# Kernel optimization log

Measured on AMD Instinct MI355X. Metric: run time of the kernel, lower is better.

## Reference

```python
import jax, jax.numpy as jnp
import numpy as np

H, W, C_IN, C_OUT, N = 512, 512, 256, 256, 65536


def setup_inputs() -> dict:
    key = jax.random.key(0)
    k1, k2, k3, k4 = jax.random.split(key, 4)
    feature = jax.random.normal(k1, (1, C_IN, H, W), dtype=jnp.float32)
    weight = jax.random.normal(k2, (C_OUT, C_IN, 3, 3), dtype=jnp.float32) * 0.05
    # base sparse locations in the unpadded map; build 3x3 neighborhood indices
    # into the PADDED ([H+2, W+2]) map, exactly like F.pad + fancy indexing.
    base_h = jax.random.randint(k3, (N,), 0, H, dtype=jnp.int32)
    base_w = jax.random.randint(k4, (N,), 0, W, dtype=jnp.int32)
    dh = jnp.repeat(jnp.arange(3, dtype=jnp.int32), 3)  # [9]: 0,0,0,1,1,1,2,2,2
    dw = jnp.tile(jnp.arange(3, dtype=jnp.int32), 3)    # [9]: 0,1,2,0,1,2,...
    h_idx = base_h[None, :] + dh[:, None]  # [9, N], values in [0, H+1]
    w_idx = base_w[None, :] + dw[:, None]  # [9, N], values in [0, W+1]
    return {"feature": feature, "weight": weight, "h_idx": h_idx, "w_idx": w_idx}


def reference(feature, weight, h_idx, w_idx):
    # feature: [1, C, H, W]; weight: [Cout, C, 3, 3]; h_idx/w_idx: [9, N]
    C = feature.shape[1]
    out_ch = weight.shape[0]
    # F.pad(feature, [1,1,1,1])[0] -> [C, H+2, W+2]
    padded = jnp.pad(feature, ((0, 0), (0, 0), (1, 1), (1, 1)))[0]
    # gather 3x3 neighborhoods at sparse locations -> [C, 9, N]
    gathered = padded[:, h_idx, w_idx]
    # .view(9*C, -1): contiguous reshape gives row index c*9 + k
    g = gathered.reshape(C * 9, -1)  # [C*9, N]
    # kernel_d2s = weight.view(out, -1): row ordering c*9 + (kh*3+kw) matches
    k2d = weight.reshape(out_ch, -1)  # [Cout, C*9]
    return k2d @ g  # [Cout, N]
```

## Files before the change

kernel.cpp:

```cpp
#include <hip/hip_runtime.h>
#include <hip/hip_bf16.h>

#define HH 512
#define WW 512
#define CIN 256
#define COUT 256
#define NPTS 65536
#define PW 514
#define NPIX (PW * PW)
#define NKT 72

typedef __bf16 bf16x8 __attribute__((ext_vector_type(8)));
typedef float f32x16 __attribute__((ext_vector_type(16)));
typedef unsigned short us8 __attribute__((ext_vector_type(8)));

static __device__ __forceinline__ unsigned short f2bf(float f) {
  unsigned u = __builtin_bit_cast(unsigned, f);
  unsigned r = u + 0x7fffu + ((u >> 16) & 1u);
  return (unsigned short)(r >> 16);
}

static __device__ __forceinline__ void gload16(const void* g, void* l) {
  __builtin_amdgcn_global_load_lds(
      (const __attribute__((address_space(1))) unsigned int*)g,
      (__attribute__((address_space(3))) unsigned int*)l, 16, 0, 0);
}

__global__ __launch_bounds__(256) void prep_weight(const float* __restrict__ w,
                                                   unsigned short* __restrict__ A) {
  int i = blockIdx.x * 256 + threadIdx.x;
  int kt = i >> 13;
  int o  = i & 8191;
  int r  = o >> 5;
  int cp = (o >> 3) & 3;
  int j  = o & 7;
  int c  = cp ^ ((r >> 1) & 3);
  int k  = kt * 32 + c * 8 + j;
  int t  = k >> 8;
  int ci = k & 255;
  A[i] = f2bf(w[r * 2304 + ci * 9 + t]);
}

__global__ __launch_bounds__(256) void border_zero(unsigned short* __restrict__ Ft) {
  int g = blockIdx.x * 256 + threadIdx.x;
  if (g >= 2052 * 32) return;
  int p = g >> 5, c = g & 31;
  int py, px;
  if (p < 514)        { py = 0;        px = p; }
  else if (p < 1028)  { py = 513;      px = p - 514; }
  else if (p < 1540)  { py = p - 1027; px = 0; }
  else                { py = p - 1539; px = 513; }
  *(us8*)&Ft[((size_t)py * PW + px) * 256 + c * 8] = (us8){0, 0, 0, 0, 0, 0, 0, 0};
}

__global__ __launch_bounds__(256) void transpose_feat(const float* __restrict__ f,
                                                      unsigned short* __restrict__ Ft) {
  __shared__ unsigned short lds[64 * 264];
  int pix0 = blockIdx.x * 64;
  int y = pix0 >> 9, x0 = pix0 & 511;
  int tid = threadIdx.x;
  int p = tid & 63;
  int cb = tid >> 6;
  const float* src = f + pix0 + p;
  for (int c8 = 0; c8 < 8; ++c8) {
    us8 v;
#pragma unroll
    for (int j = 0; j < 8; ++j) {
      int ci = cb * 64 + c8 * 8 + j;
      v[j] = f2bf(src[ci * 262144]);
    }
    *(us8*)&lds[p * 264 + cb * 64 + c8 * 8] = v;
  }
  __syncthreads();
  int cic = tid & 31;
  int pr = tid >> 5;
  for (int g = 0; g < 8; ++g) {
    int p2 = pr + g * 8;
    us8 v = *(const us8*)&lds[p2 * 264 + cic * 8];
    *(us8*)&Ft[((size_t)((y + 1) * PW + x0 + 1 + p2)) * 256 + cic * 8] = v;
  }
}

__global__ __launch_bounds__(512, 2) void gemm_gather(
    const unsigned short* __restrict__ A,
    const unsigned short* __restrict__ Ft,
    const int* __restrict__ hidx,
    const int* __restrict__ widx,
    float* __restrict__ out) {
  __shared__ unsigned short lds[73728];
  unsigned short* ldsB = lds + 24576;

  int tid = threadIdx.x;
  int lane = tid & 63, wv = tid >> 6;
  int wm = wv & 1, wn = wv >> 1;
  int n0 = blockIdx.x << 8;

  int lcB = (tid & 3) ^ ((tid >> 3) & 3);
  const unsigned short* FtQ0;
  const unsigned short* FtQ1;
  {
    int cq = tid >> 2;
    FtQ0 = Ft + (long)(hidx[n0 + cq] * PW + widx[n0 + cq]) * 256 + lcB * 8;
    FtQ1 = Ft + (long)(hidx[n0 + 128 + cq] * PW + widx[n0 + 128 + cq]) * 256 + lcB * 8;
  }

#define STAGE_A(t_, ab_)                                                      \
  do {                                                                        \
    const unsigned short* g_ = A + (size_t)(t_) * 8192 + tid * 8;             \
    unsigned short* l_ = lds + (ab_) * 8192 + tid * 8;                        \
    gload16(g_, l_);                                                          \
    gload16(g_ + 4096, l_ + 4096);                                            \
  } while (0)

#define STAGE_B(t_, bb_)                                                      \
  do {                                                                        \
    int tap_ = (t_) >> 3;                                                     \
    long off_ = (long)((tap_ / 3) * PW + (tap_ - (tap_ / 3) * 3)) * 256 +     \
                ((t_) & 7) * 32;                                              \
    unsigned short* l_ = ldsB + (bb_) * 8192 + tid * 8;                       \
    gload16(FtQ0 + off_, l_);                                                 \
    gload16(FtQ1 + off_, l_ + 4096);                                          \
  } while (0)

#define LDA(dst, ab_, kg_, mt_)                                               \
  do {                                                                        \
    int r_ = wm * 128 + (mt_) * 32 + (lane & 31);                             \
    int c_ = ((kg_) * 2 + (lane >> 5)) ^ ((r_ >> 1) & 3);                     \
    dst = *(const bf16x8*)&lds[(ab_) * 8192 + r_ * 32 + c_ * 8];              \
  } while (0)

#define LDB(dst, bb_, kg_, nt_)                                               \
  do {                                                                        \
    int col_ = wn * 64 + (nt_) * 32 + (lane & 31);                            \
    int pc_ = ((kg_) * 2 + (lane >> 5)) ^ ((col_ >> 1) & 3);                  \
    dst = *(const bf16x8*)&ldsB[(bb_) * 8192 + col_ * 32 + pc_ * 8];          \
  } while (0)

#define MFMA8(a0, a1, a2, a3, b0, b1)                                         \
  do {                                                                        \
    __builtin_amdgcn_s_setprio(1);                                            \
    acc[0][0] = __builtin_amdgcn_mfma_f32_32x32x16_bf16(a0, b0, acc[0][0], 0, 0, 0); \
    acc[0][1] = __builtin_amdgcn_mfma_f32_32x32x16_bf16(a0, b1, acc[0][1], 0, 0, 0); \
    acc[1][0] = __builtin_amdgcn_mfma_f32_32x32x16_bf16(a1, b0, acc[1][0], 0, 0, 0); \
    acc[1][1] = __builtin_amdgcn_mfma_f32_32x32x16_bf16(a1, b1, acc[1][1], 0, 0, 0); \
    acc[2][0] = __builtin_amdgcn_mfma_f32_32x32x16_bf16(a2, b0, acc[2][0], 0, 0, 0); \
    acc[2][1] = __builtin_amdgcn_mfma_f32_32x32x16_bf16(a2, b1, acc[2][1], 0, 0, 0); \
    acc[3][0] = __builtin_amdgcn_mfma_f32_32x32x16_bf16(a3, b0, acc[3][0], 0, 0, 0); \
    acc[3][1] = __builtin_amdgcn_mfma_f32_32x32x16_bf16(a3, b1, acc[3][1], 0, 0, 0); \
    __builtin_amdgcn_s_setprio(0);                                            \
  } while (0)

#define HEAD()                                                                \
  do {                                                                        \
    asm volatile("s_waitcnt lgkmcnt(0)" ::: "memory");                        \
    asm volatile("s_waitcnt vmcnt(6)" ::: "memory");                          \
    __builtin_amdgcn_s_barrier();                                             \
    __builtin_amdgcn_sched_barrier(0);                                        \
  } while (0)

  f32x16 acc[4][2];
#pragma unroll
  for (int mt = 0; mt < 4; ++mt)
#pragma unroll
    for (int nt = 0; nt < 2; ++nt)
      acc[mt][nt] = (f32x16)(0.f);

  STAGE_B(0, 0);
  STAGE_B(1, 1);
  STAGE_B(2, 2);
  STAGE_A(0, 0);
  STAGE_B(3, 3);
  STAGE_A(1, 1);
  STAGE_B(4, 4);

  for (int p = 0; p < 12; ++p) {
#pragma unroll
    for (int u = 0; u < 6; ++u) {
      int t = p * 6 + u;
      const int ab = u % 3;
      const int bb = u;
      HEAD();
      bf16x8 xa0, xa1, xa2, xa3, xb0, xb1, ya0, ya1, ya2, ya3, yb0, yb1;
      LDA(xa0, ab, 0, 0); LDA(xa1, ab, 0, 1); LDA(xa2, ab, 0, 2);
      LDA(xa3, ab, 0, 3); LDB(xb0, bb, 0, 0); LDB(xb1, bb, 0, 1);
      STAGE_A((t + 2 < NKT ? t + 2 : NKT - 1), (u + 2) % 3);
      STAGE_B((t + 5 < NKT ? t + 5 : NKT - 1), (u + 5) % 6);
      LDA(ya0, ab, 1, 0); LDA(ya1, ab, 1, 1); LDA(ya2, ab, 1, 2);
      LDA(ya3, ab, 1, 3); LDB(yb0, bb, 1, 0); LDB(yb1, bb, 1, 1);
      MFMA8(xa0, xa1, xa2, xa3, xb0, xb1);
      MFMA8(ya0, ya1, ya2, ya3, yb0, yb1);
    }
  }

#undef STAGE_A
#undef STAGE_B
#undef LDA
#undef LDB
#undef MFMA8
#undef HEAD

  int colb = n0 + wn * 64 + (lane & 31);
  int rb = wm * 128 + ((lane >> 5) << 2);
#pragma unroll
  for (int mt = 0; mt < 4; ++mt)
#pragma unroll
    for (int nt = 0; nt < 2; ++nt)
#pragma unroll
      for (int r = 0; r < 16; ++r) {
        int row = rb + mt * 32 + (r & 3) + ((r >> 2) << 3);
        out[(size_t)row * NPTS + colb + nt * 32] = acc[mt][nt][r];
      }
}

__global__ __launch_bounds__(256) void naive_conv(const float* __restrict__ f,
                                                  const float* __restrict__ w,
                                                  const int* __restrict__ hi,
                                                  const int* __restrict__ wi,
                                                  float* __restrict__ out) {
  int idx = blockIdx.x * 256 + threadIdx.x;
  int n = idx & (NPTS - 1);
  int co = idx >> 16;
  int bh = hi[n] - 1;
  int bw = wi[n] - 1;
  float acc = 0.f;
  for (int ci = 0; ci < CIN; ++ci) {
    const float* fc = f + (size_t)ci * 262144;
    const float* wc = w + (size_t)co * 2304 + ci * 9;
#pragma unroll
    for (int t = 0; t < 9; ++t) {
      int y = bh + t / 3, x = bw + t % 3;
      float v = (y >= 0 && y < 512 && x >= 0 && x < 512) ? fc[y * 512 + x] : 0.f;
      acc += wc[t] * v;
    }
  }
  out[(size_t)co * NPTS + n] = acc;
}

extern "C" void kernel_launch(void* const* d_in, const int* in_sizes, int n_in,
                              void* d_out, int out_size, void* d_ws, size_t ws_size,
                              hipStream_t stream) {
  const float* feature = (const float*)d_in[0];
  const float* weight  = (const float*)d_in[1];
  const int* hidx      = (const int*)d_in[2];
  const int* widx      = (const int*)d_in[3];
  float* out           = (float*)d_out;

  const size_t FT_OFF = 2ull * 1024 * 1024;
  const size_t FT_BYTES = (size_t)NPIX * 256 * 2;
  const size_t NEED = FT_OFF + FT_BYTES;

  if (ws_size >= NEED) {
    unsigned short* Abf = (unsigned short*)d_ws;
    unsigned short* Ft = (unsigned short*)((char*)d_ws + FT_OFF);
    prep_weight<<<(NKT * 8192) / 256, 256, 0, stream>>>(weight, Abf);
    border_zero<<<(2052 * 32 + 255) / 256, 256, 0, stream>>>(Ft);
    transpose_feat<<<262144 / 64, 256, 0, stream>>>(feature, Ft);
    gemm_gather<<<NPTS / 256, 512, 0, stream>>>(Abf, Ft, hidx, widx, out);
  } else {
    naive_conv<<<(COUT * NPTS) / 256, 256, 0, stream>>>(feature, weight, hidx, widx, out);
  }
}
```

Baseline: 176.8 us.

## Gather 128-byte pixel chunks per stage covering two k-tiles

Changes the B-operand gather so each thread loads 64 channels (128 bytes) per neighbour pixel across four pixel groups, staging two k-steps at once into a 3-deep double-width LDS ring with an 8-way XOR swizzle. The main loop is restructured into paired tiles where only even tiles issue the B gather. This aims to make scattered global reads wider and more coalesced and to reduce load instruction count. It risks weaker latency hiding because the B prefetch depth is shorter, and the unchanged vmcnt wait may not match the new uneven load pattern.

```diff
diff --git a/kernel.cpp b/kernel.cpp
--- a/kernel.cpp
+++ b/kernel.cpp
@@ -95,13 +95,14 @@
   int wm = wv & 1, wn = wv >> 1;
   int n0 = blockIdx.x << 8;
 
-  int lcB = (tid & 3) ^ ((tid >> 3) & 3);
-  const unsigned short* FtQ0;
-  const unsigned short* FtQ1;
+  int pxc = tid >> 3;
+  int lcB = (tid & 7) ^ (pxc & 7);
+  const unsigned short *FtP0, *FtP1, *FtP2, *FtP3;
   {
-    int cq = tid >> 2;
-    FtQ0 = Ft + (long)(hidx[n0 + cq] * PW + widx[n0 + cq]) * 256 + lcB * 8;
-    FtQ1 = Ft + (long)(hidx[n0 + 128 + cq] * PW + widx[n0 + 128 + cq]) * 256 + lcB * 8;
+    FtP0 = Ft + (long)(hidx[n0 + pxc] * PW + widx[n0 + pxc]) * 256 + lcB * 8;
+    FtP1 = Ft + (long)(hidx[n0 + 64 + pxc] * PW + widx[n0 + 64 + pxc]) * 256 + lcB * 8;
+    FtP2 = Ft + (long)(hidx[n0 + 128 + pxc] * PW + widx[n0 + 128 + pxc]) * 256 + lcB * 8;
+    FtP3 = Ft + (long)(hidx[n0 + 192 + pxc] * PW + widx[n0 + 192 + pxc]) * 256 + lcB * 8;
   }
 
 #define STAGE_A(t_, ab_)                                                      \
@@ -112,14 +113,16 @@
     gload16(g_ + 4096, l_ + 4096);                                            \
   } while (0)
 
-#define STAGE_B(t_, bb_)                                                      \
-  do {                                                                        \
-    int tap_ = (t_) >> 3;                                                     \
+#define STAGE_BP(q_, bb_)                                                     \
+  do {                                                                        \
+    int tap_ = (q_) >> 2;                                                     \
     long off_ = (long)((tap_ / 3) * PW + (tap_ - (tap_ / 3) * 3)) * 256 +     \
-                ((t_) & 7) * 32;                                              \
-    unsigned short* l_ = ldsB + (bb_) * 8192 + tid * 8;                       \
-    gload16(FtQ0 + off_, l_);                                                 \
-    gload16(FtQ1 + off_, l_ + 4096);                                          \
+                ((q_) & 3) * 64;                                              \
+    unsigned short* l_ = ldsB + (bb_) * 16384 + tid * 8;                      \
+    gload16(FtP0 + off_, l_);                                                 \
+    gload16(FtP1 + off_, l_ + 4096);                                          \
+    gload16(FtP2 + off_, l_ + 8192);                                          \
+    gload16(FtP3 + off_, l_ + 12288);                                         \
   } while (0)
 
 #define LDA(dst, ab_, kg_, mt_)                                               \
@@ -129,11 +132,11 @@
     dst = *(const bf16x8*)&lds[(ab_) * 8192 + r_ * 32 + c_ * 8];              \
   } while (0)
 
-#define LDB(dst, bb_, kg_, nt_)                                               \
+#define LDB(dst, bb_, s_, kg_, nt_)                                           \
   do {                                                                        \
     int col_ = wn * 64 + (nt_) * 32 + (lane & 31);                            \
-    int pc_ = ((kg_) * 2 + (lane >> 5)) ^ ((col_ >> 1) & 3);                  \
-    dst = *(const bf16x8*)&ldsB[(bb_) * 8192 + col_ * 32 + pc_ * 8];          \
+    int ph_ = ((s_) * 4 + (kg_) * 2 + (lane >> 5)) ^ (col_ & 7);              \
+    dst = *(const bf16x8*)&ldsB[(bb_) * 16384 + col_ * 64 + ph_ * 8];         \
   } while (0)
 
 #define MFMA8(a0, a1, a2, a3, b0, b1)                                         \
@@ -158,6 +161,19 @@
     __builtin_amdgcn_sched_barrier(0);                                        \
   } while (0)
 
+#define TILE(ab_, bb_, s_, ...)                                               \
+  do {                                                                        \
+    HEAD();                                                                   \
+    bf16x8 xa0, xa1, xa2, xa3, xb0, xb1, ya0, ya1, ya2, ya3, yb0, yb1;        \
+    LDA(xa0, ab_, 0, 0); LDA(xa1, ab_, 0, 1); LDA(xa2, ab_, 0, 2);            \
+    LDA(xa3, ab_, 0, 3); LDB(xb0, bb_, s_, 0, 0); LDB(xb1, bb_, s_, 0, 1);    \
+    __VA_ARGS__;                                                              \
+    LDA(ya0, ab_, 1, 0); LDA(ya1, ab_, 1, 1); LDA(ya2, ab_, 1, 2);            \
+    LDA(ya3, ab_, 1, 3); LDB(yb0, bb_, s_, 1, 0); LDB(yb1, bb_, s_, 1, 1);    \
+    MFMA8(xa0, xa1, xa2, xa3, xb0, xb1);                                      \
+    MFMA8(ya0, ya1, ya2, ya3, yb0, yb1);                                      \
+  } while (0)
+
   f32x16 acc[4][2];
 #pragma unroll
   for (int mt = 0; mt < 4; ++mt)
@@ -165,39 +181,31 @@
     for (int nt = 0; nt < 2; ++nt)
       acc[mt][nt] = (f32x16)(0.f);
 
-  STAGE_B(0, 0);
-  STAGE_B(1, 1);
-  STAGE_B(2, 2);
+  STAGE_BP(0, 0);
   STAGE_A(0, 0);
-  STAGE_B(3, 3);
   STAGE_A(1, 1);
-  STAGE_B(4, 4);
-
-  for (int p = 0; p < 12; ++p) {
-#pragma unroll
-    for (int u = 0; u < 6; ++u) {
-      int t = p * 6 + u;
-      const int ab = u % 3;
-      const int bb = u;
-      HEAD();
-      bf16x8 xa0, xa1, xa2, xa3, xb0, xb1, ya0, ya1, ya2, ya3, yb0, yb1;
-      LDA(xa0, ab, 0, 0); LDA(xa1, ab, 0, 1); LDA(xa2, ab, 0, 2);
-      LDA(xa3, ab, 0, 3); LDB(xb0, bb, 0, 0); LDB(xb1, bb, 0, 1);
-      STAGE_A((t + 2 < NKT ? t + 2 : NKT - 1), (u + 2) % 3);
-      STAGE_B((t + 5 < NKT ? t + 5 : NKT - 1), (u + 5) % 6);
-      LDA(ya0, ab, 1, 0); LDA(ya1, ab, 1, 1); LDA(ya2, ab, 1, 2);
-      LDA(ya3, ab, 1, 3); LDB(yb0, bb, 1, 0); LDB(yb1, bb, 1, 1);
-      MFMA8(xa0, xa1, xa2, xa3, xb0, xb1);
-      MFMA8(ya0, ya1, ya2, ya3, yb0, yb1);
+  STAGE_BP(1, 1);
+
+  for (int P3 = 0; P3 < 12; ++P3) {
+#pragma unroll
+    for (int v = 0; v < 3; ++v) {
+      int q = P3 * 3 + v;
+      int t = 2 * q;
+      TILE((2 * v) % 3, v, 0,
+           STAGE_A((t + 2 < NKT ? t + 2 : NKT - 1), (2 * v + 2) % 3);
+           STAGE_BP((q + 2 < 36 ? q + 2 : 35), (v + 2) % 3));
+      TILE((2 * v + 1) % 3, v, 1,
+           STAGE_A((t + 3 < NKT ? t + 3 : NKT - 1), (2 * v) % 3));
     }
   }
 
 #undef STAGE_A
-#undef STAGE_B
+#undef STAGE_BP
 #undef LDA
 #undef LDB
 #undef MFMA8
 #undef HEAD
+#undef TILE
 
   int colb = n0 + wn * 64 + (lane & 31);
   int rb = wm * 128 + ((lane >> 5) << 2);
```

Result: faster. 171.7 us (-2.9%).
